# Kernel optimization log

Hardware: AMD Instinct MI355X
Metric: run time of the kernel (lower is better)

The kernel has to match this reference:

```python
import jax, jax.numpy as jnp
import numpy as np

N_POINTS = 4096
N_PROJS = 2000


def setup_inputs() -> dict:
    key = jax.random.key(0)
    k1, k2, k3 = jax.random.split(key, 3)
    Xs = jax.random.normal(k1, (N_POINTS, 3), dtype=jnp.float32)
    Xt = jax.random.normal(k2, (N_POINTS, 3), dtype=jnp.float32)
    Us = jax.random.normal(k3, (N_PROJS, 3, 2), dtype=jnp.float32)
    return {"Xs": Xs, "Xt": Xt, "Us": Us}


def _project_to_circle(X, Us):
    # X: [n, d], Us: [P, d, 2] -> angles in [0, 1): [P, n]
    Xp = jnp.einsum('pdk,nd->pnk', Us, X)  # [P, n, 2]
    nrm = jnp.sqrt(jnp.sum(Xp * Xp, axis=-1, keepdims=True))
    Xp = Xp / jnp.maximum(nrm, 1e-12)  # F.normalize
    return (jnp.arctan2(-Xp[..., 1], -Xp[..., 0]) + np.pi) / (2 * np.pi)


def _emd1d_circle_p1(u_values, v_values):
    # Circular W1 via level-median (Delon et al.). u,v: [P, n], [P, m]
    P, n = u_values.shape
    m = v_values.shape[-1]
    dt = u_values.dtype
    u_w = jnp.full((P, n), 1.0 / n, dtype=dt)
    v_w = jnp.full((P, m), 1.0 / m, dtype=dt)
    us = jnp.sort(u_values, axis=-1)
    vs = jnp.sort(v_values, axis=-1)
    vals = jnp.concatenate([us, vs], axis=-1)            # [P, n+m]
    sorter = jnp.argsort(vals, axis=-1)
    vals_sorted = jnp.take_along_axis(vals, sorter, axis=-1)
    w_cat = jnp.concatenate([u_w, -v_w], axis=-1)
    cdf_diff = jnp.cumsum(jnp.take_along_axis(w_cat, sorter, axis=-1), axis=-1)
    cdf_sorter = jnp.argsort(cdf_diff, axis=-1)
    cdf_diff_sorted = jnp.take_along_axis(cdf_diff, cdf_sorter, axis=-1)
    vals_pad = jnp.concatenate([vals_sorted, jnp.ones((P, 1), dtype=dt)], axis=-1)
    delta = vals_pad[..., 1:] - vals_pad[..., :-1]
    weight_sorted = jnp.take_along_axis(delta, cdf_sorter, axis=-1)
    sum_weights = jnp.cumsum(weight_sorted, axis=-1) - 0.5
    sum_weights = jnp.where(sum_weights < 0, jnp.inf, sum_weights)
    inds = jnp.argmin(sum_weights, axis=-1)
    levMed = jnp.take_along_axis(cdf_diff_sorted, inds[:, None], axis=-1)  # [P, 1]
    return jnp.sum(delta * jnp.abs(cdf_diff - levMed), axis=-1)  # [P]


def reference(Xs, Xt, Us):
    Xps = _project_to_circle(Xs, Us)  # [P, n]
    Xpt = _project_to_circle(Xt, Us)  # [P, m]
    w1 = _emd1d_circle_p1(Xps, Xpt)
    return jnp.mean(w1)
```

## Files before the change

### kernel.cpp

```cpp
#include <hip/hip_runtime.h>
#include <math.h>

#define NPTS   4096
#define NPROJ  2000
#define NB     512
#define NMERGE 8192
#define VPT    16

__device__ __forceinline__ int sw(int i) {
    return (i & ~31) | ((i + (i >> 5)) & 31);
}

__device__ __forceinline__ void local_merge(float v[VPT], bool asc) {
    #pragma unroll
    for (int j = 8; j >= 1; j >>= 1) {
        #pragma unroll
        for (int e = 0; e < VPT; ++e) {
            if ((e & j) == 0) {
                float a = v[e], b = v[e | j];
                float mn = fminf(a, b), mx = fmaxf(a, b);
                v[e]     = asc ? mn : mx;
                v[e | j] = asc ? mx : mn;
            }
        }
    }
}

__global__ __launch_bounds__(NB) void swd_kernel(
    const float* __restrict__ Xs, const float* __restrict__ Xt,
    const float* __restrict__ Us, float* __restrict__ out)
{
    __shared__ float keys[NMERGE];

    const int tid  = threadIdx.x;
    const int arr  = tid >> 8;
    const int c    = tid & 255;
    const int lane = tid & 63;
    const int wid  = tid >> 6;
    const int p    = blockIdx.x;

    const float u00 = Us[p*6+0], u01 = Us[p*6+1];
    const float u10 = Us[p*6+2], u11 = Us[p*6+3];
    const float u20 = Us[p*6+4], u21 = Us[p*6+5];

    const float pi_f   = 3.14159265358979323846f;
    const float inv2pi = 0.15915494309189535f;

    const float* __restrict__ X = arr ? Xt : Xs;

    float v[VPT];
    {
        const float4* X4 = (const float4*)(X + c * (VPT * 3));
        #pragma unroll
        for (int t = 0; t < 4; ++t) {
            float4 q0 = X4[t*3+0], q1 = X4[t*3+1], q2 = X4[t*3+2];
            #define ANG(x,y,z) ((atan2f(-((x)*u01+(y)*u11+(z)*u21), \
                                        -((x)*u00+(y)*u10+(z)*u20)) + pi_f) * inv2pi)
            v[t*4+0] = ANG(q0.x, q0.y, q0.z);
            v[t*4+1] = ANG(q0.w, q1.x, q1.y);
            v[t*4+2] = ANG(q1.z, q1.w, q2.x);
            v[t*4+3] = ANG(q2.y, q2.z, q2.w);
            #undef ANG
        }
    }

    #pragma unroll
    for (int k = 2; k <= 8; k <<= 1) {
        #pragma unroll
        for (int j = k >> 1; j >= 1; j >>= 1) {
            #pragma unroll
            for (int e = 0; e < VPT; ++e) {
                if ((e & j) == 0) {
                    bool asc = ((e & k) == 0);
                    float a = v[e], b = v[e | j];
                    float mn = fminf(a, b), mx = fmaxf(a, b);
                    v[e]     = asc ? mn : mx;
                    v[e | j] = asc ? mx : mn;
                }
            }
        }
    }

    local_merge(v, (c & 1) == 0);

    #pragma unroll
    for (int k = 32; k <= 1024; k <<= 1) {
        bool asc = ((c & (k >> 4)) == 0);
        #pragma unroll
        for (int d = k >> 5; d >= 1; d >>= 1) {
            bool keepmin = (((c & d) == 0) == asc);
            #pragma unroll
            for (int e = 0; e < VPT; ++e) {
                float o = __shfl_xor(v[e], d, 64);
                v[e] = keepmin ? fminf(v[e], o) : fmaxf(v[e], o);
            }
        }
        local_merge(v, asc);
    }

    #define LDS_XCHG(PXOR, KEEPMIN_EXPR)                                   \
    {                                                                      \
        _Pragma("unroll")                                                  \
        for (int e = 0; e < VPT; ++e) keys[sw(tid * VPT + e)] = v[e];      \
        __syncthreads();                                                   \
        const int pbase = (tid ^ (PXOR)) * VPT;                            \
        const bool keepmin = (KEEPMIN_EXPR);                               \
        _Pragma("unroll")                                                  \
        for (int e = 0; e < VPT; ++e) {                                    \
            float o = keys[sw(pbase + e)];                                 \
            v[e] = keepmin ? fminf(v[e], o) : fmaxf(v[e], o);              \
        }                                                                  \
        __syncthreads();                                                   \
    }

    {
        bool asc = ((c & 128) == 0);
        LDS_XCHG(64, ((c & 64) == 0) == asc);
        #pragma unroll
        for (int d = 32; d >= 1; d >>= 1) {
            bool keepmin = (((c & d) == 0) == asc);
            #pragma unroll
            for (int e = 0; e < VPT; ++e) {
                float o = __shfl_xor(v[e], d, 64);
                v[e] = keepmin ? fminf(v[e], o) : fmaxf(v[e], o);
            }
        }
        local_merge(v, asc);
    }

    LDS_XCHG(128, (c & 128) == 0);
    LDS_XCHG(64,  (c & 64) == 0);
    #pragma unroll
    for (int d = 32; d >= 1; d >>= 1) {
        bool keepmin = ((c & d) == 0);
        #pragma unroll
        for (int e = 0; e < VPT; ++e) {
            float o = __shfl_xor(v[e], d, 64);
            v[e] = keepmin ? fminf(v[e], o) : fmaxf(v[e], o);
        }
    }
    local_merge(v, true);
    #undef LDS_XCHG

    #pragma unroll
    for (int e = 0; e < VPT; ++e) keys[sw(tid * VPT + e)] = v[e];
    __syncthreads();

    int c_init;
    int offmin = 32, offmax = -32;
    float offf[VPT];
    {
        const int d0 = tid * VPT;
        int lo = d0 > NPTS ? d0 - NPTS : 0;
        int hi = d0 < NPTS ? d0 : NPTS;
        while (lo < hi) {
            int mid = (lo + hi) >> 1;
            if (keys[sw(mid)] <= keys[sw(NPTS + (d0 - 1 - mid))]) lo = mid + 1; else hi = mid;
        }
        int i = lo, j = d0 - lo;
        c_init = i - j;
        const float FMAXV = 3.402823466e+38f;
        float cu = (i < NPTS) ? keys[sw(i)] : FMAXV;
        float cv = (j < NPTS) ? keys[sw(NPTS + j)] : FMAXV;
        #pragma unroll
        for (int s = 0; s < VPT; ++s) {
            float cur;
            if (cu <= cv) { cur = cu; ++i; cu = (i < NPTS) ? keys[sw(i)] : FMAXV; }
            else          { cur = cv; ++j; cv = (j < NPTS) ? keys[sw(NPTS + j)] : FMAXV; }
            float nxt = fminf(cu, cv);
            if (nxt == FMAXV) nxt = 1.0f;
            v[s] = nxt - cur;
            int off = (i - j) - c_init;
            offmin = min(offmin, off);
            offmax = max(offmax, off);
            offf[s] = (float)off;
        }
    }

    __syncthreads();
    int*   ired = (int*)keys;
    float* red  = keys + 16;

    int cmn = c_init + offmin, cmx = c_init + offmax;
    #pragma unroll
    for (int o = 32; o >= 1; o >>= 1) {
        cmn = min(cmn, __shfl_xor(cmn, o, 64));
        cmx = max(cmx, __shfl_xor(cmx, o, 64));
    }
    if (lane == 0) { ired[wid] = cmn; ired[8 + wid] = cmx; }
    __syncthreads();
    {
        int a0 = min(min(ired[0], ired[1]), min(ired[2], ired[3]));
        int a1 = min(min(ired[4], ired[5]), min(ired[6], ired[7]));
        cmn = min(a0, a1);
        int b0 = max(max(ired[8], ired[9]),  max(ired[10], ired[11]));
        int b1 = max(max(ired[12], ired[13]), max(ired[14], ired[15]));
        cmx = max(b0, b1);
    }

    int lo_c = cmn - 1, hi_c = cmx;
    int it = 0;
    #pragma unroll 1
    while (hi_c - lo_c > 1) {
        const int mid = (lo_c + hi_c) >> 1;
        const float thrf = (float)(mid - c_init);
        float s_loc = 0.0f;
        #pragma unroll
        for (int s = 0; s < VPT; ++s)
            s_loc += (offf[s] <= thrf) ? v[s] : 0.0f;
        #pragma unroll
        for (int o = 32; o >= 1; o >>= 1) s_loc += __shfl_down(s_loc, o, 64);
        if (lane == 0) red[it * 8 + wid] = s_loc;
        __syncthreads();
        float S = 0.0f;
        #pragma unroll
        for (int w = 0; w < 8; ++w) S += red[it * 8 + w];
        if (S >= 0.5f) hi_c = mid; else lo_c = mid;
        ++it;
    }
    const int cstar = hi_c;

    float part = 0.0f;
    {
        const float thrf = (float)(cstar - c_init);
        #pragma unroll
        for (int s = 0; s < VPT; ++s)
            part += v[s] * fabsf(offf[s] - thrf);
    }
    #pragma unroll
    for (int o = 32; o >= 1; o >>= 1) part += __shfl_down(part, o, 64);
    if (lane == 0) red[15 * 8 + wid] = part;
    __syncthreads();
    if (tid == 0) {
        float w1 = 0.0f;
        #pragma unroll
        for (int w = 0; w < 8; ++w) w1 += red[15 * 8 + w];
        w1 *= (1.0f / 4096.0f);
        atomicAdd(out, w1 * (1.0f / (float)NPROJ));
    }
}

extern "C" void kernel_launch(void* const* d_in, const int* in_sizes, int n_in,
                              void* d_out, int out_size, void* d_ws, size_t ws_size,
                              hipStream_t stream) {
    const float* Xs = (const float*)d_in[0];
    const float* Xt = (const float*)d_in[1];
    const float* Us = (const float*)d_in[2];
    float* out = (float*)d_out;

    hipMemsetAsync(out, 0, sizeof(float), stream);
    swd_kernel<<<NPROJ, NB, 0, stream>>>(Xs, Xt, Us, out);
}
```

Baseline: 227.0 us.

## Replace final bitonic merge stages with merge-path merges in LDS

The last two bitonic merge levels of the per-array 4096-element sort, which used LDS exchanges plus shuffle and register stages, are replaced by merge-path merges. Each thread binary-searches its split point in two sorted runs and sequentially merges 16 outputs. Runs of 1024 are now all ascending, so adjacent pairs can be merged directly. This cuts the compare-exchange work and the syncs, at the cost of data-dependent LDS reads and branch divergence in the serial merge loop.

```diff
diff --git a/kernel.cpp b/kernel.cpp
--- a/kernel.cpp
+++ b/kernel.cpp
@@ -85,7 +85,7 @@
 
     #pragma unroll
     for (int k = 32; k <= 1024; k <<= 1) {
-        bool asc = ((c & (k >> 4)) == 0);
+        bool asc = (k == 1024) || ((c & (k >> 4)) == 0);
         #pragma unroll
         for (int d = k >> 5; d >= 1; d >>= 1) {
             bool keepmin = (((c & d) == 0) == asc);
@@ -98,53 +98,42 @@
         local_merge(v, asc);
     }
 
-    #define LDS_XCHG(PXOR, KEEPMIN_EXPR)                                   \
-    {                                                                      \
-        _Pragma("unroll")                                                  \
-        for (int e = 0; e < VPT; ++e) keys[sw(tid * VPT + e)] = v[e];      \
-        __syncthreads();                                                   \
-        const int pbase = (tid ^ (PXOR)) * VPT;                            \
-        const bool keepmin = (KEEPMIN_EXPR);                               \
-        _Pragma("unroll")                                                  \
-        for (int e = 0; e < VPT; ++e) {                                    \
-            float o = keys[sw(pbase + e)];                                 \
-            v[e] = keepmin ? fminf(v[e], o) : fmaxf(v[e], o);              \
-        }                                                                  \
-        __syncthreads();                                                   \
-    }
-
-    {
-        bool asc = ((c & 128) == 0);
-        LDS_XCHG(64, ((c & 64) == 0) == asc);
-        #pragma unroll
-        for (int d = 32; d >= 1; d >>= 1) {
-            bool keepmin = (((c & d) == 0) == asc);
-            #pragma unroll
-            for (int e = 0; e < VPT; ++e) {
-                float o = __shfl_xor(v[e], d, 64);
-                v[e] = keepmin ? fminf(v[e], o) : fmaxf(v[e], o);
-            }
-        }
-        local_merge(v, asc);
-    }
-
-    LDS_XCHG(128, (c & 128) == 0);
-    LDS_XCHG(64,  (c & 64) == 0);
-    #pragma unroll
-    for (int d = 32; d >= 1; d >>= 1) {
-        bool keepmin = ((c & d) == 0);
-        #pragma unroll
-        for (int e = 0; e < VPT; ++e) {
-            float o = __shfl_xor(v[e], d, 64);
-            v[e] = keepmin ? fminf(v[e], o) : fmaxf(v[e], o);
-        }
-    }
-    local_merge(v, true);
-    #undef LDS_XCHG
-
     #pragma unroll
     for (int e = 0; e < VPT; ++e) keys[sw(tid * VPT + e)] = v[e];
     __syncthreads();
+
+    #define MERGE_ROUND(L, AB, DD)                                          \
+    {                                                                       \
+        const int Ab = (AB);                                                \
+        const int Bb = Ab + (L);                                            \
+        const int dd = (DD);                                                \
+        int lo = dd > (L) ? dd - (L) : 0;                                   \
+        int hi = dd < (L) ? dd : (L);                                       \
+        while (lo < hi) {                                                   \
+            int mid = (lo + hi) >> 1;                                       \
+            if (keys[sw(Ab + mid)] <= keys[sw(Bb + (dd - 1 - mid))])        \
+                lo = mid + 1; else hi = mid;                                \
+        }                                                                   \
+        int i = lo, j = dd - lo;                                            \
+        const float INFV = __builtin_inff();                                \
+        float cu = (i < (L)) ? keys[sw(Ab + i)] : INFV;                     \
+        float cv = (j < (L)) ? keys[sw(Bb + j)] : INFV;                     \
+        _Pragma("unroll")                                                   \
+        for (int s = 0; s < VPT; ++s) {                                     \
+            bool take = (cu <= cv);                                         \
+            v[s] = fminf(cu, cv);                                           \
+            if (take) { ++i; cu = (i < (L)) ? keys[sw(Ab + i)] : INFV; }    \
+            else      { ++j; cv = (j < (L)) ? keys[sw(Bb + j)] : INFV; }    \
+        }                                                                   \
+        __syncthreads();                                                    \
+        _Pragma("unroll")                                                   \
+        for (int e = 0; e < VPT; ++e) keys[sw(tid * VPT + e)] = v[e];       \
+        __syncthreads();                                                    \
+    }
+
+    MERGE_ROUND(1024, arr * 4096 + (c >> 7) * 2048, (c & 127) * VPT)
+    MERGE_ROUND(2048, arr * 4096, c * VPT)
+    #undef MERGE_ROUND
 
     int c_init;
     int offmin = 32, offmax = -32;
```

Result: faster. 220.9 us (-2.7%).
